# Kernel tuning notes

Measured on AMD Instinct MI355X. Metric: run time of the kernel, lower is better.

## Reference

```python
import jax, jax.numpy as jnp
import numpy as np

HID = 64
L = 5
N_NODES = 50000
N_EDGES = 1600000
N_GRAPHS = 4
EPS = 1e-5


def _ln(h, g, b):
    m = jnp.mean(h, axis=-1, keepdims=True)
    v = jnp.mean((h - m) ** 2, axis=-1, keepdims=True)
    return (h - m) * jax.lax.rsqrt(v + EPS) * g + b


def _lin_init(key, fan_in, fan_out):
    return jax.random.normal(key, (fan_in, fan_out), jnp.float32) / np.sqrt(fan_in)


def setup_inputs() -> dict:
    key = jax.random.key(0)
    ks = jax.random.split(key, 24)
    inp = {}
    inp['x'] = jax.random.normal(ks[0], (N_NODES, 8), jnp.float32)
    inp['edge_index'] = jax.random.randint(ks[1], (2, N_EDGES), 0, N_NODES)
    inp['edge_attr'] = jax.random.normal(ks[2], (N_EDGES, 5), jnp.float32)
    inp['batch'] = jnp.sort(jax.random.randint(ks[3], (N_NODES,), 0, N_GRAPHS))
    inp['case_params'] = jax.random.normal(ks[4], (N_GRAPHS, 4), jnp.float32)
    inp['bc_params'] = jax.random.normal(ks[5], (N_GRAPHS, 4), jnp.float32)
    # encoder
    inp['enc_W1'] = _lin_init(ks[6], 16, HID); inp['enc_b1'] = jnp.zeros((HID,))
    inp['enc_W2'] = _lin_init(ks[7], HID, HID); inp['enc_b2'] = jnp.zeros((HID,))
    inp['enc_g'] = jnp.ones((HID,)); inp['enc_be'] = jnp.zeros((HID,))
    # processor (stacked over L layers)
    ek = jax.random.split(ks[8], L); nk = jax.random.split(ks[9], L)
    ek2 = jax.random.split(ks[10], L); nk2 = jax.random.split(ks[11], L)
    inp['eW1'] = jnp.stack([_lin_init(ek[i], 2 * HID + 5, HID) for i in range(L)])
    inp['eb1'] = jnp.zeros((L, HID))
    inp['eW2'] = jnp.stack([_lin_init(ek2[i], HID, HID) for i in range(L)])
    inp['eb2'] = jnp.zeros((L, HID))
    inp['eg'] = jnp.ones((L, HID)); inp['ebe'] = jnp.zeros((L, HID))
    inp['nW1'] = jnp.stack([_lin_init(nk[i], 2 * HID, HID) for i in range(L)])
    inp['nb1'] = jnp.zeros((L, HID))
    inp['nW2'] = jnp.stack([_lin_init(nk2[i], HID, HID) for i in range(L)])
    inp['nb2'] = jnp.zeros((L, HID))
    inp['ng'] = jnp.ones((L, HID)); inp['nbe'] = jnp.zeros((L, HID))
    # decoders
    inp['dlW1'] = _lin_init(ks[12], HID, HID); inp['dlb1'] = jnp.zeros((HID,))
    inp['dlW2'] = _lin_init(ks[13], HID, 6); inp['dlb2'] = jnp.zeros((6,))
    inp['dgW1'] = _lin_init(ks[14], HID, HID // 2); inp['dgb1'] = jnp.zeros((HID // 2,))
    inp['dgW2'] = _lin_init(ks[15], HID // 2, 4); inp['dgb2'] = jnp.zeros((4,))
    return inp


def reference(x, edge_index, edge_attr, batch, case_params, bc_params,
              enc_W1, enc_b1, enc_W2, enc_b2, enc_g, enc_be,
              eW1, eb1, eW2, eb2, eg, ebe,
              nW1, nb1, nW2, nb2, ng, nbe,
              dlW1, dlb1, dlW2, dlb2, dgW1, dgb1, dgW2, dgb2):
    n_nodes = x.shape[0]
    n_graphs = case_params.shape[0]
    silu = jax.nn.silu
    # input concat: node feats + per-graph globals gathered by batch index
    gv = jnp.concatenate([case_params, bc_params], axis=1)  # [B, 8]
    h = jnp.concatenate([x, gv[batch]], axis=1)             # [N, 16]
    # encoder
    h = _ln(silu(h @ enc_W1 + enc_b1) @ enc_W2 + enc_b2, enc_g, enc_be)
    src, dst = edge_index[0], edge_index[1]  # PyG: x_j = src, x_i = dst
    n_layers = eW1.shape[0]
    for l in range(n_layers):
        xi = h[dst]  # [E, H] target
        xj = h[src]  # [E, H] source
        m = jnp.concatenate([xi, xj, edge_attr], axis=1)  # [E, 2H+5]
        m = _ln(silu(m @ eW1[l] + eb1[l]) @ eW2[l] + eb2[l], eg[l], ebe[l])
        agg = jax.ops.segment_sum(m, dst, num_segments=n_nodes)  # scatter-add
        t = jnp.concatenate([h, agg], axis=1)  # [N, 2H]
        h = h + _ln(silu(t @ nW1[l] + nb1[l]) @ nW2[l] + nb2[l], ng[l], nbe[l])
    out_local = silu(h @ dlW1 + dlb1) @ dlW2 + dlb2  # [N, 6]
    cnt = jax.ops.segment_sum(jnp.ones((n_nodes,), h.dtype), batch, num_segments=n_graphs)
    pooled = jax.ops.segment_sum(h, batch, num_segments=n_graphs) / jnp.maximum(cnt, 1.0)[:, None]
    out_global = silu(pooled @ dgW1 + dgb1) @ dgW2 + dgb2  # [B, 4]
    return (out_local, out_global)
```

## Files before the change

kernel.cpp:

```cpp
#include <hip/hip_runtime.h>
#include <cmath>

constexpr int NN = 50000;
constexpr int NE = 1600000;
constexpr int H  = 64;
constexpr int NL = 5;
constexpr int NG = 4;
constexpr int EIN = 2 * H + 5;
constexpr int NIN = 2 * H;

typedef short bf16x8 __attribute__((ext_vector_type(8)));
typedef float f32x4  __attribute__((ext_vector_type(4)));

__device__ __forceinline__ float silu_f(float x) {
    return x / (1.0f + __expf(-x));
}

__device__ __forceinline__ unsigned int f2bf(float f) {
    unsigned int u = __float_as_uint(f);
    u += 0x7fffu + ((u >> 16) & 1u);
    return u >> 16;
}
__device__ __forceinline__ unsigned int pack_bf16x2(float x, float y) {
    unsigned int r;
    asm("v_cvt_pk_bf16_f32 %0, %1, %2" : "=v"(r) : "v"(x), "v"(y));
    return r;
}

template <int CTRL>
__device__ __forceinline__ int dpp_i(int old, int v) {
    return __builtin_amdgcn_update_dpp(old, v, CTRL, 0xF, 0xF, false);
}

__global__ __launch_bounds__(256) void degree_kernel(
    const int* __restrict__ ei, int* __restrict__ deg)
{
    int e = blockIdx.x * 256 + threadIdx.x;
    if (e < NE) atomicAdd(&deg[ei[NE + e]], 1);
}

__global__ __launch_bounds__(1024) void scan1_kernel(
    const int* __restrict__ deg, int* __restrict__ off, int* __restrict__ bsum)
{
    __shared__ int sh[1024];
    const int tid = threadIdx.x;
    int i = blockIdx.x * 1024 + tid;
    int v = (i < NN) ? deg[i] : 0;
    sh[tid] = v;
    __syncthreads();
    for (int d = 1; d < 1024; d <<= 1) {
        int t = (tid >= d) ? sh[tid - d] : 0;
        __syncthreads();
        sh[tid] += t;
        __syncthreads();
    }
    if (i < NN) off[i] = sh[tid] - v;
    if (tid == 1023) bsum[blockIdx.x] = sh[1023];
}

__global__ __launch_bounds__(64) void scan2_kernel(
    const int* __restrict__ bsum, int* __restrict__ bbase, int nb)
{
    int lane = threadIdx.x;
    int v = (lane < nb) ? bsum[lane] : 0;
    int orig = v;
    for (int d = 1; d < 64; d <<= 1) {
        int t = __shfl_up(v, d);
        if (lane >= d) v += t;
    }
    bbase[lane] = v - orig;
}

__global__ __launch_bounds__(1024) void scan3_kernel(
    int* __restrict__ off, const int* __restrict__ bbase,
    int* __restrict__ cursor)
{
    int i = blockIdx.x * 1024 + threadIdx.x;
    if (i < NN) {
        int o = off[i] + bbase[blockIdx.x];
        off[i] = o;
        cursor[i] = o;
        if (i == NN - 1) off[NN] = NE;
    }
}

__global__ __launch_bounds__(256) void scatter_kernel(
    const int* __restrict__ ei, int* __restrict__ cursor,
    int* __restrict__ sidx, int* __restrict__ sdst, int* __restrict__ ssrc)
{
    int e = blockIdx.x * 256 + threadIdx.x;
    if (e < NE) {
        int d = ei[NE + e];
        int p = atomicAdd(&cursor[d], 1);
        sidx[p] = e;
        sdst[p] = d;
        ssrc[p] = ei[e];
    }
}

__global__ __launch_bounds__(256) void ea_pack_kernel(
    const float* __restrict__ ea, const int* __restrict__ sidx,
    uint4* __restrict__ ea_pk)
{
    int p = blockIdx.x * 256 + threadIdx.x;
    if (p < NE) {
        const float* s = ea + (size_t)sidx[p] * 5;
        uint4 v;
        v.x = pack_bf16x2(s[0], s[1]);
        v.y = pack_bf16x2(s[2], s[3]);
        v.z = pack_bf16x2(s[4], 0.0f);
        v.w = 0u;
        ea_pk[p] = v;
    }
}

__global__ __launch_bounds__(256) void pack_weights_kernel(
    const float* __restrict__ eW1, const float* __restrict__ eW2,
    const float* __restrict__ nW1, const float* __restrict__ nW2,
    const float* __restrict__ dlW1, const float* __restrict__ dlW2,
    short* __restrict__ eW1pk, short* __restrict__ eW2pk,
    short* __restrict__ nW1pk, short* __restrict__ nW2pk,
    short* __restrict__ dlW1pk, short* __restrict__ dlW2pk)
{
    int l = blockIdx.y;
    int t = blockIdx.x * 256 + threadIdx.x;
    if (t < 10240) {
        int j = t & 7, lane = (t >> 3) & 63, mt = (t >> 9) & 3, ks = t >> 11;
        int k  = ks * 32 + (lane >> 4) * 8 + j;
        int ch = mt * 16 + (lane & 15);
        float v = (k < EIN) ? eW1[(size_t)l * EIN * H + k * H + ch] : 0.0f;
        eW1pk[(size_t)l * 10240 + t] = (short)f2bf(v);
    } else if (t < 14336) {
        int t2 = t - 10240;
        int j = t2 & 7, lane = (t2 >> 3) & 63, mt = (t2 >> 9) & 3, ks = t2 >> 11;
        int k = ks * 32 + (lane >> 4) * 8 + j;
        int ch = mt * 16 + (lane & 15);
        eW2pk[(size_t)l * 4096 + t2] = (short)f2bf(eW2[(size_t)l * H * H + k * H + ch]);
    } else if (t < 22528) {
        int t3 = t - 14336;
        int j = t3 & 7, lane = (t3 >> 3) & 63, mt = (t3 >> 9) & 3, ks = t3 >> 11;
        int k = ks * 32 + (lane >> 4) * 8 + j;
        int ch = mt * 16 + (lane & 15);
        nW1pk[(size_t)l * 8192 + t3] = (short)f2bf(nW1[(size_t)l * NIN * H + k * H + ch]);
    } else if (t < 26624) {
        int t4 = t - 22528;
        int j = t4 & 7, lane = (t4 >> 3) & 63, mt = (t4 >> 9) & 3, ks = t4 >> 11;
        int k = ks * 32 + (lane >> 4) * 8 + j;
        int ch = mt * 16 + (lane & 15);
        nW2pk[(size_t)l * 4096 + t4] = (short)f2bf(nW2[(size_t)l * H * H + k * H + ch]);
    } else if (t < 30720) {
        if (l == 0) {
            int t5 = t - 26624;
            int j = t5 & 7, lane = (t5 >> 3) & 63, mt = (t5 >> 9) & 3, ks = t5 >> 11;
            int k = ks * 32 + (lane >> 4) * 8 + j;
            int ch = mt * 16 + (lane & 15);
            dlW1pk[t5] = (short)f2bf(dlW1[k * H + ch]);
        }
    } else if (t < 31744) {
        if (l == 0) {
            int t6 = t - 30720;
            int j = t6 & 7, lane = (t6 >> 3) & 63, ks = t6 >> 9;
            int k = ks * 32 + (lane >> 4) * 8 + j;
            int m = lane & 15;
            float v = (m < 6) ? dlW2[k * 6 + m] : 0.0f;
            dlW2pk[t6] = (short)f2bf(v);
        }
    }
}

__global__ __launch_bounds__(256) void encoder_kernel(
    const float* __restrict__ x, const int* __restrict__ batch,
    const float* __restrict__ case_p, const float* __restrict__ bc_p,
    const float* __restrict__ W1, const float* __restrict__ b1,
    const float* __restrict__ W2, const float* __restrict__ b2,
    const float* __restrict__ g, const float* __restrict__ be,
    float* __restrict__ h, unsigned int* __restrict__ h2)
{
    __shared__ float in_sh[64 * 17];
    __shared__ float m1_sh[64 * 65];
    __shared__ float red_sh[2 * 4 * 64];
    const int lane = threadIdx.x & 63;
    const int w    = threadIdx.x >> 6;
    const int wb   = __builtin_amdgcn_readfirstlane(w * 16);
    const int n0   = blockIdx.x * 64;

    for (int i = 0; i < 16; ++i) {
        int slot = w * 16 + i;
        int n = n0 + slot;
        if (n < NN && lane < 16) {
            float v;
            if (lane < 8) v = x[n * 8 + lane];
            else {
                int b = batch[n];
                v = (lane < 12) ? case_p[b * 4 + (lane - 8)]
                                : bc_p[b * 4 + (lane - 12)];
            }
            in_sh[slot * 17 + lane] = v;
        }
    }
    __syncthreads();

    float acc[16];
#pragma unroll
    for (int c = 0; c < 16; ++c) acc[c] = b1[wb + c];
    for (int k = 0; k < 16; ++k) {
        float a = in_sh[lane * 17 + k];
        const float4* wr = (const float4*)(W1 + k * 64 + wb);
        float4 w0 = wr[0], w1 = wr[1], w2 = wr[2], w3 = wr[3];
        acc[0]  = fmaf(a, w0.x, acc[0]);  acc[1]  = fmaf(a, w0.y, acc[1]);
        acc[2]  = fmaf(a, w0.z, acc[2]);  acc[3]  = fmaf(a, w0.w, acc[3]);
        acc[4]  = fmaf(a, w1.x, acc[4]);  acc[5]  = fmaf(a, w1.y, acc[5]);
        acc[6]  = fmaf(a, w1.z, acc[6]);  acc[7]  = fmaf(a, w1.w, acc[7]);
        acc[8]  = fmaf(a, w2.x, acc[8]);  acc[9]  = fmaf(a, w2.y, acc[9]);
        acc[10] = fmaf(a, w2.z, acc[10]); acc[11] = fmaf(a, w2.w, acc[11]);
        acc[12] = fmaf(a, w3.x, acc[12]); acc[13] = fmaf(a, w3.y, acc[13]);
        acc[14] = fmaf(a, w3.z, acc[14]); acc[15] = fmaf(a, w3.w, acc[15]);
    }
#pragma unroll
    for (int c = 0; c < 16; ++c) m1_sh[lane * 65 + wb + c] = silu_f(acc[c]);
    __syncthreads();

    float acc2[16];
#pragma unroll
    for (int c = 0; c < 16; ++c) acc2[c] = b2[wb + c];
    for (int k = 0; k < 64; ++k) {
        float a = m1_sh[lane * 65 + k];
        const float4* wr = (const float4*)(W2 + k * 64 + wb);
        float4 w0 = wr[0], w1 = wr[1], w2 = wr[2], w3 = wr[3];
        acc2[0]  = fmaf(a, w0.x, acc2[0]);  acc2[1]  = fmaf(a, w0.y, acc2[1]);
        acc2[2]  = fmaf(a, w0.z, acc2[2]);  acc2[3]  = fmaf(a, w0.w, acc2[3]);
        acc2[4]  = fmaf(a, w1.x, acc2[4]);  acc2[5]  = fmaf(a, w1.y, acc2[5]);
        acc2[6]  = fmaf(a, w1.z, acc2[6]);  acc2[7]  = fmaf(a, w1.w, acc2[7]);
        acc2[8]  = fmaf(a, w2.x, acc2[8]);  acc2[9]  = fmaf(a, w2.y, acc2[9]);
        acc2[10] = fmaf(a, w2.z, acc2[10]); acc2[11] = fmaf(a, w2.w, acc2[11]);
        acc2[12] = fmaf(a, w3.x, acc2[12]); acc2[13] = fmaf(a, w3.y, acc2[13]);
        acc2[14] = fmaf(a, w3.z, acc2[14]); acc2[15] = fmaf(a, w3.w, acc2[15]);
    }

    float s1 = 0.f, s2 = 0.f;
#pragma unroll
    for (int c = 0; c < 16; ++c) { s1 += acc2[c]; s2 += acc2[c] * acc2[c]; }
    red_sh[w * 64 + lane] = s1;
    red_sh[256 + w * 64 + lane] = s2;
    __syncthreads();
    float t1 = 0.f, t2 = 0.f;
#pragma unroll
    for (int j = 0; j < 4; ++j) {
        t1 += red_sh[j * 64 + lane];
        t2 += red_sh[256 + j * 64 + lane];
    }
    float mean = t1 * (1.0f / 64.0f);
    float var  = t2 * (1.0f / 64.0f) - mean * mean;
    float rstd = rsqrtf(var + 1e-5f);

    int n = n0 + lane;
    if (n < NN) {
        float vals[16];
#pragma unroll
        for (int c = 0; c < 16; ++c) {
            int ch = wb + c;
            vals[c] = (acc2[c] - mean) * rstd * g[ch] + be[ch];
            h[n * 64 + ch] = vals[c];
        }
        uint4 p0, p1;
        p0.x = pack_bf16x2(vals[0], vals[1]);   p0.y = pack_bf16x2(vals[2], vals[3]);
        p0.z = pack_bf16x2(vals[4], vals[5]);   p0.w = pack_bf16x2(vals[6], vals[7]);
        p1.x = pack_bf16x2(vals[8], vals[9]);   p1.y = pack_bf16x2(vals[10], vals[11]);
        p1.z = pack_bf16x2(vals[12], vals[13]); p1.w = pack_bf16x2(vals[14], vals[15]);
        *(uint4*)(h2 + (size_t)n * 32 + w * 8)     = p0;
        *(uint4*)(h2 + (size_t)n * 32 + w * 8 + 4) = p1;
    }
}

__global__ __launch_bounds__(256, 7) void edge_kernel(
    const unsigned int* __restrict__ h2,
    const int* __restrict__ sdst, const int* __restrict__ ssrc,
    const uint4* __restrict__ ea_pk,
    const short* __restrict__ W1pk, const float* __restrict__ b1,
    const short* __restrict__ W2pk, const float* __restrict__ b2,
    const float* __restrict__ g, const float* __restrict__ be,
    float* __restrict__ agg)
{
    __shared__ unsigned int lds[4 * 576];
    const int lane = threadIdx.x & 63;
    const int w    = threadIdx.x >> 6;
    const int quad = lane >> 4;
    const int l15  = lane & 15;
    const int tile = (blockIdx.x & 7) * 3125 + (blockIdx.x >> 3);
    const int e0   = tile * 64 + w * 16;
    unsigned int* MID = lds + w * 576;

    const int d_l = sdst[e0 + l15];
    const int s_l = ssrc[e0 + l15];

    union { uint4 u; bf16x8 b; } eacv;
    eacv.u = ea_pk[e0 + l15];
    const bf16x8 zfrag = {0, 0, 0, 0, 0, 0, 0, 0};
    const bf16x8 ks4frag = (quad == 0) ? eacv.b : zfrag;

    const unsigned int* drow = h2 + (size_t)d_l * 32 + quad * 4;
    const unsigned int* srow = h2 + (size_t)s_l * 32 + quad * 4;
    union { uint4 u; bf16x8 b; } bfA, bfB, bfC, bfD;
    bfA.u = *(const uint4*)(drow);
    bfB.u = *(const uint4*)(drow + 16);
    bfC.u = *(const uint4*)(srow);
    bfD.u = *(const uint4*)(srow + 16);

    f32x4 acc1[4] = {{0,0,0,0},{0,0,0,0},{0,0,0,0},{0,0,0,0}};
#define G1_STEP(KS, BFRAG)                                                    \
    {                                                                         \
        const short* apk = W1pk + (size_t)((KS) * 4) * 512 + lane * 8;        \
        _Pragma("unroll")                                                     \
        for (int mt = 0; mt < 4; ++mt) {                                      \
            bf16x8 afrag = *(const bf16x8*)(apk + mt * 512);                  \
            acc1[mt] = __builtin_amdgcn_mfma_f32_16x16x32_bf16(               \
                afrag, BFRAG, acc1[mt], 0, 0, 0);                             \
        }                                                                     \
    }
    G1_STEP(0, bfA.b)
    G1_STEP(1, bfB.b)
    G1_STEP(2, bfC.b)
    G1_STEP(3, bfD.b)
    G1_STEP(4, ks4frag)
#undef G1_STEP

#pragma unroll
    for (int mt = 0; mt < 4; ++mt) {
        int ch0 = mt * 16 + quad * 4;
        float v0 = silu_f(acc1[mt][0] + b1[ch0 + 0]);
        float v1 = silu_f(acc1[mt][1] + b1[ch0 + 1]);
        float v2 = silu_f(acc1[mt][2] + b1[ch0 + 2]);
        float v3 = silu_f(acc1[mt][3] + b1[ch0 + 3]);
        uint2 pk;
        pk.x = pack_bf16x2(v0, v1);
        pk.y = pack_bf16x2(v2, v3);
        *(uint2*)(MID + l15 * 36 + mt * 8 + quad * 2) = pk;
    }

    f32x4 acc2[4] = {{0,0,0,0},{0,0,0,0},{0,0,0,0},{0,0,0,0}};
    const unsigned int* mrow = MID + l15 * 36;
    for (int ks = 0; ks < 2; ++ks) {
        bf16x8 bfrag = *(const bf16x8*)(mrow + ks * 16 + quad * 4);
        const short* apk = W2pk + (size_t)(ks * 4) * 512 + lane * 8;
#pragma unroll
        for (int mt = 0; mt < 4; ++mt) {
            bf16x8 afrag = *(const bf16x8*)(apk + mt * 512);
            acc2[mt] = __builtin_amdgcn_mfma_f32_16x16x32_bf16(
                afrag, bfrag, acc2[mt], 0, 0, 0);
        }
    }

    float vals[16];
    float s1 = 0.f, s2 = 0.f;
#pragma unroll
    for (int mt = 0; mt < 4; ++mt) {
#pragma unroll
        for (int r = 0; r < 4; ++r) {
            int ch = mt * 16 + quad * 4 + r;
            float vv = acc2[mt][r] + b2[ch];
            vals[mt * 4 + r] = vv;
            s1 += vv; s2 += vv * vv;
        }
    }
    s1 += __shfl_xor(s1, 16); s1 += __shfl_xor(s1, 32);
    s2 += __shfl_xor(s2, 16); s2 += __shfl_xor(s2, 32);
    float mean = s1 * (1.0f / 64.0f);
    float var  = s2 * (1.0f / 64.0f) - mean * mean;
    float rstd = rsqrtf(var + 1e-5f);
#pragma unroll
    for (int mt = 0; mt < 4; ++mt) {
#pragma unroll
        for (int r = 0; r < 4; ++r) {
            int ch = mt * 16 + quad * 4 + r;
            vals[mt * 4 + r] = (vals[mt * 4 + r] - mean) * rstd * g[ch] + be[ch];
        }
    }

#define SEG_STEP(CTRL)                                                        \
    {                                                                         \
        int d_up = dpp_i<CTRL>(-1, d_l);                                      \
        float msk = (d_up == d_l) ? 1.0f : 0.0f;                              \
        _Pragma("unroll")                                                     \
        for (int c = 0; c < 16; ++c) {                                        \
            float vu = __int_as_float(dpp_i<CTRL>(0, __float_as_int(vals[c])));\
            vals[c] = fmaf(vu, msk, vals[c]);                                 \
        }                                                                     \
    }
    SEG_STEP(0x111)
    SEG_STEP(0x112)
    SEG_STEP(0x114)
    SEG_STEP(0x118)
#undef SEG_STEP
    int d_next = dpp_i<0x101>(-1, d_l);
    bool last = (d_next != d_l);
    if (last) {
#pragma unroll
        for (int mt = 0; mt < 4; ++mt) {
#pragma unroll
            for (int r = 0; r < 4; ++r) {
                int ch = mt * 16 + quad * 4 + r;
                atomicAdd(&agg[(size_t)d_l * 64 + ch], vals[mt * 4 + r]);
            }
        }
    }
}

__global__ __launch_bounds__(256, 6) void node_kernel(
    float* __restrict__ h, unsigned int* __restrict__ h2,
    const float* __restrict__ agg,
    const short* __restrict__ W1pk, const float* __restrict__ b1,
    const short* __restrict__ W2pk, const float* __restrict__ b2,
    const float* __restrict__ g, const float* __restrict__ be)
{
    __shared__ unsigned int lds[4 * 576];
    const int lane = threadIdx.x & 63;
    const int w    = threadIdx.x >> 6;
    const int quad = lane >> 4;
    const int l15  = lane & 15;
    const int n0   = blockIdx.x * 64 + w * 16;
    unsigned int* MID = lds + w * 576;

    int n_l = n0 + l15; if (n_l >= NN) n_l = NN - 1;

    const unsigned int* nrow = h2 + (size_t)n_l * 32 + quad * 4;
    union { uint4 u; bf16x8 b; } bfA, bfB;
    bfA.u = *(const uint4*)(nrow);
    bfB.u = *(const uint4*)(nrow + 16);
    const float* ap = agg + (size_t)n_l * 64 + quad * 8;
    float4 a0 = *(const float4*)(ap);
    float4 a1 = *(const float4*)(ap + 4);
    float4 a2 = *(const float4*)(ap + 32);
    float4 a3 = *(const float4*)(ap + 36);
    union { unsigned int u[4]; bf16x8 b; } bfC, bfD;
    bfC.u[0] = pack_bf16x2(a0.x, a0.y); bfC.u[1] = pack_bf16x2(a0.z, a0.w);
    bfC.u[2] = pack_bf16x2(a1.x, a1.y); bfC.u[3] = pack_bf16x2(a1.z, a1.w);
    bfD.u[0] = pack_bf16x2(a2.x, a2.y); bfD.u[1] = pack_bf16x2(a2.z, a2.w);
    bfD.u[2] = pack_bf16x2(a3.x, a3.y); bfD.u[3] = pack_bf16x2(a3.z, a3.w);

    f32x4 acc1[4] = {{0,0,0,0},{0,0,0,0},{0,0,0,0},{0,0,0,0}};
#define G1_STEP(KS, BFRAG)                                                    \
    {                                                                         \
        const short* apk = W1pk + (size_t)((KS) * 4) * 512 + lane * 8;        \
        _Pragma("unroll")                                                     \
        for (int mt = 0; mt < 4; ++mt) {                                      \
            bf16x8 afrag = *(const bf16x8*)(apk + mt * 512);                  \
            acc1[mt] = __builtin_amdgcn_mfma_f32_16x16x32_bf16(               \
                afrag, BFRAG, acc1[mt], 0, 0, 0);                             \
        }                                                                     \
    }
    G1_STEP(0, bfA.b)
    G1_STEP(1, bfB.b)
    G1_STEP(2, bfC.b)
    G1_STEP(3, bfD.b)
#undef G1_STEP

#pragma unroll
    for (int mt = 0; mt < 4; ++mt) {
        int ch0 = mt * 16 + quad * 4;
        float v0 = silu_f(acc1[mt][0] + b1[ch0 + 0]);
        float v1 = silu_f(acc1[mt][1] + b1[ch0 + 1]);
        float v2 = silu_f(acc1[mt][2] + b1[ch0 + 2]);
        float v3 = silu_f(acc1[mt][3] + b1[ch0 + 3]);
        uint2 pk;
        pk.x = pack_bf16x2(v0, v1);
        pk.y = pack_bf16x2(v2, v3);
        *(uint2*)(MID + l15 * 36 + mt * 8 + quad * 2) = pk;
    }

    f32x4 acc2[4] = {{0,0,0,0},{0,0,0,0},{0,0,0,0},{0,0,0,0}};
    const unsigned int* mrow = MID + l15 * 36;
    for (int ks = 0; ks < 2; ++ks) {
        bf16x8 bfrag = *(const bf16x8*)(mrow + ks * 16 + quad * 4);
        const short* apk = W2pk + (size_t)(ks * 4) * 512 + lane * 8;
#pragma unroll
        for (int mt = 0; mt < 4; ++mt) {
            bf16x8 afrag = *(const bf16x8*)(apk + mt * 512);
            acc2[mt] = __builtin_amdgcn_mfma_f32_16x16x32_bf16(
                afrag, bfrag, acc2[mt], 0, 0, 0);
        }
    }

    float vals[16];
    float s1 = 0.f, s2 = 0.f;
#pragma unroll
    for (int mt = 0; mt < 4; ++mt) {
#pragma unroll
        for (int r = 0; r < 4; ++r) {
            int ch = mt * 16 + quad * 4 + r;
            float vv = acc2[mt][r] + b2[ch];
            vals[mt * 4 + r] = vv;
            s1 += vv; s2 += vv * vv;
        }
    }
    s1 += __shfl_xor(s1, 16); s1 += __shfl_xor(s1, 32);
    s2 += __shfl_xor(s2, 16); s2 += __shfl_xor(s2, 32);
    float mean = s1 * (1.0f / 64.0f);
    float var  = s2 * (1.0f / 64.0f) - mean * mean;
    float rstd = rsqrtf(var + 1e-5f);

    int n = n0 + l15;
    if (n < NN) {
#pragma unroll
        for (int mt = 0; mt < 4; ++mt) {
            int ch0 = mt * 16 + quad * 4;
            float4 hv = *(const float4*)(h + (size_t)n * 64 + ch0);
            float o0 = hv.x + (vals[mt*4+0] - mean) * rstd * g[ch0+0] + be[ch0+0];
            float o1 = hv.y + (vals[mt*4+1] - mean) * rstd * g[ch0+1] + be[ch0+1];
            float o2 = hv.z + (vals[mt*4+2] - mean) * rstd * g[ch0+2] + be[ch0+2];
            float o3 = hv.w + (vals[mt*4+3] - mean) * rstd * g[ch0+3] + be[ch0+3];
            float4 st = {o0, o1, o2, o3};
            *(float4*)(h + (size_t)n * 64 + ch0) = st;
            uint2 pk;
            pk.x = pack_bf16x2(o0, o1);
            pk.y = pack_bf16x2(o2, o3);
            *(uint2*)(h2 + (size_t)n * 32 + mt * 8 + quad * 2) = pk;
        }
    }
}

__global__ __launch_bounds__(256, 7) void dec_local_kernel(
    const unsigned int* __restrict__ h2,
    const short* __restrict__ W1pk, const float* __restrict__ b1,
    const short* __restrict__ W2pk, const float* __restrict__ b2,
    float* __restrict__ out)
{
    __shared__ unsigned int lds[4 * 576];
    const int lane = threadIdx.x & 63;
    const int w    = threadIdx.x >> 6;
    const int quad = lane >> 4;
    const int l15  = lane & 15;
    const int n0   = blockIdx.x * 64 + w * 16;
    unsigned int* MID = lds + w * 576;

    int n_l = n0 + l15; if (n_l >= NN) n_l = NN - 1;
    const unsigned int* nrow = h2 + (size_t)n_l * 32 + quad * 4;
    union { uint4 u; bf16x8 b; } bfA, bfB;
    bfA.u = *(const uint4*)(nrow);
    bfB.u = *(const uint4*)(nrow + 16);

    f32x4 acc1[4] = {{0,0,0,0},{0,0,0,0},{0,0,0,0},{0,0,0,0}};
#define G1_STEP(KS, BFRAG)                                                    \
    {                                                                         \
        const short* apk = W1pk + (size_t)((KS) * 4) * 512 + lane * 8;        \
        _Pragma("unroll")                                                     \
        for (int mt = 0; mt < 4; ++mt) {                                      \
            bf16x8 afrag = *(const bf16x8*)(apk + mt * 512);                  \
            acc1[mt] = __builtin_amdgcn_mfma_f32_16x16x32_bf16(               \
                afrag, BFRAG, acc1[mt], 0, 0, 0);                             \
        }                                                                     \
    }
    G1_STEP(0, bfA.b)
    G1_STEP(1, bfB.b)
#undef G1_STEP

#pragma unroll
    for (int mt = 0; mt < 4; ++mt) {
        int ch0 = mt * 16 + quad * 4;
        float v0 = silu_f(acc1[mt][0] + b1[ch0 + 0]);
        float v1 = silu_f(acc1[mt][1] + b1[ch0 + 1]);
        float v2 = silu_f(acc1[mt][2] + b1[ch0 + 2]);
        float v3 = silu_f(acc1[mt][3] + b1[ch0 + 3]);
        uint2 pk;
        pk.x = pack_bf16x2(v0, v1);
        pk.y = pack_bf16x2(v2, v3);
        *(uint2*)(MID + l15 * 36 + mt * 8 + quad * 2) = pk;
    }

    f32x4 acc2 = {0, 0, 0, 0};
    const unsigned int* mrow = MID + l15 * 36;
    for (int ks = 0; ks < 2; ++ks) {
        bf16x8 bfrag = *(const bf16x8*)(mrow + ks * 16 + quad * 4);
        bf16x8 afrag = *(const bf16x8*)(W2pk + (size_t)ks * 512 + lane * 8);
        acc2 = __builtin_amdgcn_mfma_f32_16x16x32_bf16(afrag, bfrag, acc2, 0, 0, 0);
    }

    int n = n0 + l15;
    if (n < NN && quad < 2) {
#pragma unroll
        for (int r = 0; r < 4; ++r) {
            int ch = quad * 4 + r;
            if (ch < 6) out[(size_t)n * 6 + ch] = acc2[r] + b2[ch];
        }
    }
}

__global__ __launch_bounds__(256) void pool_kernel(
    const float* __restrict__ h, const int* __restrict__ batch,
    float* __restrict__ pooled, float* __restrict__ cnt)
{
    const int c   = threadIdx.x & 63;
    const int rep = blockIdx.x * 4 + (threadIdx.x >> 6);
    float acc[NG] = {0.f, 0.f, 0.f, 0.f};
    float cl[NG]  = {0.f, 0.f, 0.f, 0.f};
    for (int n = rep; n < NN; n += 1024) {
        int b = batch[n];
        float v = h[n * 64 + c];
#pragma unroll
        for (int gph = 0; gph < NG; ++gph) {
            if (b == gph) { acc[gph] += v; cl[gph] += 1.0f; }
        }
    }
#pragma unroll
    for (int gph = 0; gph < NG; ++gph) {
        atomicAdd(&pooled[gph * 64 + c], acc[gph]);
        if (c == 0) atomicAdd(&cnt[gph], cl[gph]);
    }
}

__global__ __launch_bounds__(256) void dec_global_kernel(
    const float* __restrict__ pooled, const float* __restrict__ cnt,
    const float* __restrict__ W1, const float* __restrict__ b1,
    const float* __restrict__ W2, const float* __restrict__ b2,
    float* __restrict__ out)
{
    __shared__ float mid_sh[4][32];
    const int lane = threadIdx.x & 63;
    const int gph  = threadIdx.x >> 6;
    float inv = 1.0f / fmaxf(cnt[gph], 1.0f);
    if (lane < 32) {
        float a = b1[lane];
        for (int k = 0; k < 64; ++k)
            a = fmaf(pooled[gph * 64 + k] * inv, W1[k * 32 + lane], a);
        mid_sh[gph][lane] = silu_f(a);
    }
    __syncthreads();
    if (lane < 4) {
        float o = b2[lane];
        for (int k = 0; k < 32; ++k)
            o = fmaf(mid_sh[gph][k], W2[k * 4 + lane], o);
        out[gph * 4 + lane] = o;
    }
}

extern "C" void kernel_launch(void* const* d_in, const int* in_sizes, int n_in,
                              void* d_out, int out_size, void* d_ws, size_t ws_size,
                              hipStream_t stream)
{
    const float* x      = (const float*)d_in[0];
    const int*   ei     = (const int*)  d_in[1];
    const float* ea     = (const float*)d_in[2];
    const int*   batch  = (const int*)  d_in[3];
    const float* case_p = (const float*)d_in[4];
    const float* bc_p   = (const float*)d_in[5];
    const float* enc_W1 = (const float*)d_in[6];
    const float* enc_b1 = (const float*)d_in[7];
    const float* enc_W2 = (const float*)d_in[8];
    const float* enc_b2 = (const float*)d_in[9];
    const float* enc_g  = (const float*)d_in[10];
    const float* enc_be = (const float*)d_in[11];
    const float* eW1    = (const float*)d_in[12];
    const float* eb1    = (const float*)d_in[13];
    const float* eW2    = (const float*)d_in[14];
    const float* eb2    = (const float*)d_in[15];
    const float* eg     = (const float*)d_in[16];
    const float* ebe    = (const float*)d_in[17];
    const float* nW1    = (const float*)d_in[18];
    const float* nb1    = (const float*)d_in[19];
    const float* nW2    = (const float*)d_in[20];
    const float* nb2    = (const float*)d_in[21];
    const float* ng     = (const float*)d_in[22];
    const float* nbe    = (const float*)d_in[23];
    const float* dlW1   = (const float*)d_in[24];
    const float* dlb1   = (const float*)d_in[25];
    const float* dlW2   = (const float*)d_in[26];
    const float* dlb2   = (const float*)d_in[27];
    const float* dgW1   = (const float*)d_in[28];
    const float* dgb1   = (const float*)d_in[29];
    const float* dgW2   = (const float*)d_in[30];
    const float* dgb2   = (const float*)d_in[31];

    float* out = (float*)d_out;

    char* ws = (char*)d_ws;
    size_t off_b = 0;
    auto alloc = [&](size_t bytes) {
        void* p = ws + off_b;
        off_b = (off_b + bytes + 255) & ~(size_t)255;
        return p;
    };
    const size_t hBytes = (size_t)NN * H * sizeof(float);
    float*        h      = (float*)alloc(hBytes);
    float*        agg    = (float*)alloc(hBytes);
    unsigned int* h2     = (unsigned int*)alloc((size_t)NN * 32 * 4);
    float*        pooled = (float*)alloc(256 * sizeof(float));
    float*        cnt    = (float*)alloc(4 * sizeof(float));
    int*          deg    = (int*)alloc((NN + 1) * sizeof(int));
    int*          offs   = (int*)alloc((NN + 1) * sizeof(int));
    int*          cursor = (int*)alloc((NN + 1) * sizeof(int));
    int*          bsum   = (int*)alloc(64 * sizeof(int));
    int*          bbase  = (int*)alloc(64 * sizeof(int));
    int*          sidx   = (int*)alloc((size_t)NE * sizeof(int));
    int*          sdst   = (int*)alloc((size_t)NE * sizeof(int));
    int*          ssrc   = (int*)alloc((size_t)NE * sizeof(int));
    uint4*        ea_pk  = (uint4*)alloc((size_t)NE * sizeof(uint4));
    short*        eW1pk  = (short*)alloc((size_t)NL * 10240 * sizeof(short));
    short*        eW2pk  = (short*)alloc((size_t)NL * 4096 * sizeof(short));
    short*        nW1pk  = (short*)alloc((size_t)NL * 8192 * sizeof(short));
    short*        nW2pk  = (short*)alloc((size_t)NL * 4096 * sizeof(short));
    short*        dlW1pk = (short*)alloc(4096 * sizeof(short));
    short*        dlW2pk = (short*)alloc(1024 * sizeof(short));

    hipMemsetAsync(pooled, 0, (256 + 4 + 64) * sizeof(float), stream);
    hipMemsetAsync(deg, 0, (NN + 1) * sizeof(int), stream);

    const int NB = (NN + 1023) / 1024;
    degree_kernel<<<(NE + 255) / 256, 256, 0, stream>>>(ei, deg);
    scan1_kernel<<<NB, 1024, 0, stream>>>(deg, offs, bsum);
    scan2_kernel<<<1, 64, 0, stream>>>(bsum, bbase, NB);
    scan3_kernel<<<NB, 1024, 0, stream>>>(offs, bbase, cursor);
    scatter_kernel<<<(NE + 255) / 256, 256, 0, stream>>>(ei, cursor, sidx, sdst, ssrc);
    ea_pack_kernel<<<(NE + 255) / 256, 256, 0, stream>>>(ea, sidx, ea_pk);
    pack_weights_kernel<<<dim3(124, NL), 256, 0, stream>>>(
        eW1, eW2, nW1, nW2, dlW1, dlW2,
        eW1pk, eW2pk, nW1pk, nW2pk, dlW1pk, dlW2pk);

    const int nodeBlocks = (NN + 63) / 64;
    encoder_kernel<<<nodeBlocks, 256, 0, stream>>>(
        x, batch, case_p, bc_p, enc_W1, enc_b1, enc_W2, enc_b2, enc_g, enc_be,
        h, h2);

    for (int l = 0; l < NL; ++l) {
        hipMemsetAsync(agg, 0, hBytes, stream);
        edge_kernel<<<NE / 64, 256, 0, stream>>>(
            h2, sdst, ssrc, ea_pk,
            eW1pk + (size_t)l * 10240, eb1 + l * H,
            eW2pk + (size_t)l * 4096,  eb2 + l * H,
            eg + l * H, ebe + l * H, agg);
        node_kernel<<<nodeBlocks, 256, 0, stream>>>(
            h, h2, agg,
            nW1pk + (size_t)l * 8192, nb1 + l * H,
            nW2pk + (size_t)l * 4096, nb2 + l * H,
            ng + l * H, nbe + l * H);
    }

    dec_local_kernel<<<nodeBlocks, 256, 0, stream>>>(
        h2, dlW1pk, dlb1, dlW2pk, dlb2, out);
    pool_kernel<<<256, 256, 0, stream>>>(h, batch, pooled, cnt);
    dec_global_kernel<<<1, 256, 0, stream>>>(pooled, cnt, dgW1, dgb1, dgW2, dgb2,
                                             out + (size_t)NN * 6);
}
```

Baseline: 1.590 ms.

## Stage edge/node MLP weights in LDS and make edge kernel persistent

The edge kernel now launches 800 blocks of 512 threads. Each block first copies the packed W1/W2 weights, biases and LayerNorm params into LDS, then loops its 8 waves over 125 sixteen-edge tiles, instead of launching one block per 64 edges that reads weights from global memory. The node kernel gets the same LDS staging with 512-thread blocks covering 128 nodes. The aim is to cut repeated global/L2 weight-fragment loads for the MFMA A-operands and spread the staging cost over many tiles. In exchange it uses about 37KB of LDS per block, which may limit occupancy, and adds a block-level sync.

```diff
diff --git a/kernel.cpp b/kernel.cpp
--- a/kernel.cpp
+++ b/kernel.cpp
@@ -272,7 +272,7 @@
     }
 }
 
-__global__ __launch_bounds__(256, 7) void edge_kernel(
+__global__ __launch_bounds__(512, 6) void edge_kernel(
     const unsigned int* __restrict__ h2,
     const int* __restrict__ sdst, const int* __restrict__ ssrc,
     const uint4* __restrict__ ea_pk,
@@ -281,145 +281,199 @@
     const float* __restrict__ g, const float* __restrict__ be,
     float* __restrict__ agg)
 {
-    __shared__ unsigned int lds[4 * 576];
-    const int lane = threadIdx.x & 63;
-    const int w    = threadIdx.x >> 6;
+    __shared__ uint4 w1s4[1280];
+    __shared__ uint4 w2s4[512];
+    __shared__ float b1s[64], b2s[64], gs[64], bes[64];
+    __shared__ unsigned int mids[8 * 576];
+
+    const int tid  = threadIdx.x;
+    const int lane = tid & 63;
+    const int w    = tid >> 6;
     const int quad = lane >> 4;
     const int l15  = lane & 15;
-    const int tile = (blockIdx.x & 7) * 3125 + (blockIdx.x >> 3);
-    const int e0   = tile * 64 + w * 16;
-    unsigned int* MID = lds + w * 576;
-
-    const int d_l = sdst[e0 + l15];
-    const int s_l = ssrc[e0 + l15];
-
-    union { uint4 u; bf16x8 b; } eacv;
-    eacv.u = ea_pk[e0 + l15];
+
+    {
+        const uint4* s1 = (const uint4*)W1pk;
+        for (int i = tid; i < 1280; i += 512) w1s4[i] = s1[i];
+        const uint4* s2 = (const uint4*)W2pk;
+        w2s4[tid] = s2[tid];
+        if (tid < 64) {
+            b1s[tid] = b1[tid];
+            b2s[tid] = b2[tid];
+            gs[tid]  = g[tid];
+            bes[tid] = be[tid];
+        }
+    }
+    __syncthreads();
+
+    const short* w1s = (const short*)w1s4;
+    const short* w2s = (const short*)w2s4;
+    unsigned int* MID = mids + w * 576;
     const bf16x8 zfrag = {0, 0, 0, 0, 0, 0, 0, 0};
-    const bf16x8 ks4frag = (quad == 0) ? eacv.b : zfrag;
-
-    const unsigned int* drow = h2 + (size_t)d_l * 32 + quad * 4;
-    const unsigned int* srow = h2 + (size_t)s_l * 32 + quad * 4;
-    union { uint4 u; bf16x8 b; } bfA, bfB, bfC, bfD;
-    bfA.u = *(const uint4*)(drow);
-    bfB.u = *(const uint4*)(drow + 16);
-    bfC.u = *(const uint4*)(srow);
-    bfD.u = *(const uint4*)(srow + 16);
-
-    f32x4 acc1[4] = {{0,0,0,0},{0,0,0,0},{0,0,0,0},{0,0,0,0}};
+
+    const int blk   = (blockIdx.x & 7) * 100 + (blockIdx.x >> 3);
+    const int wbase = blk * 125;
+
+    for (int W = wbase + w; W < wbase + 125; W += 8) {
+        const int eI = W * 16 + l15;
+        const int d_l = sdst[eI];
+        const int s_l = ssrc[eI];
+        union { uint4 u; bf16x8 b; } eacv;
+        eacv.u = ea_pk[eI];
+        bf16x8 ks4frag = (quad == 0) ? eacv.b : zfrag;
+
+        const unsigned int* drow = h2 + (size_t)d_l * 32 + quad * 4;
+        const unsigned int* srow = h2 + (size_t)s_l * 32 + quad * 4;
+        union { uint4 u; bf16x8 b; } bfA, bfB, bfC, bfD;
+        bfA.u = *(const uint4*)(drow);
+        bfB.u = *(const uint4*)(drow + 16);
+        bfC.u = *(const uint4*)(srow);
+        bfD.u = *(const uint4*)(srow + 16);
+
+        f32x4 acc1[4] = {{0,0,0,0},{0,0,0,0},{0,0,0,0},{0,0,0,0}};
 #define G1_STEP(KS, BFRAG)                                                    \
-    {                                                                         \
-        const short* apk = W1pk + (size_t)((KS) * 4) * 512 + lane * 8;        \
-        _Pragma("unroll")                                                     \
-        for (int mt = 0; mt < 4; ++mt) {                                      \
-            bf16x8 afrag = *(const bf16x8*)(apk + mt * 512);                  \
-            acc1[mt] = __builtin_amdgcn_mfma_f32_16x16x32_bf16(               \
-                afrag, BFRAG, acc1[mt], 0, 0, 0);                             \
-        }                                                                     \
-    }
-    G1_STEP(0, bfA.b)
-    G1_STEP(1, bfB.b)
-    G1_STEP(2, bfC.b)
-    G1_STEP(3, bfD.b)
-    G1_STEP(4, ks4frag)
+        {                                                                     \
+            const short* apk = w1s + (KS) * 4 * 512 + lane * 8;               \
+            _Pragma("unroll")                                                 \
+            for (int mt = 0; mt < 4; ++mt) {                                  \
+                bf16x8 afrag = *(const bf16x8*)(apk + mt * 512);              \
+                acc1[mt] = __builtin_amdgcn_mfma_f32_16x16x32_bf16(           \
+                    afrag, BFRAG, acc1[mt], 0, 0, 0);                         \
+            }                                                                 \
+        }
+        G1_STEP(0, bfA.b)
+        G1_STEP(1, bfB.b)
+        G1_STEP(2, bfC.b)
+        G1_STEP(3, bfD.b)
+        G1_STEP(4, ks4frag)
 #undef G1_STEP
 
 #pragma unroll
-    for (int mt = 0; mt < 4; ++mt) {
-        int ch0 = mt * 16 + quad * 4;
-        float v0 = silu_f(acc1[mt][0] + b1[ch0 + 0]);
-        float v1 = silu_f(acc1[mt][1] + b1[ch0 + 1]);
-        float v2 = silu_f(acc1[mt][2] + b1[ch0 + 2]);
-        float v3 = silu_f(acc1[mt][3] + b1[ch0 + 3]);
-        uint2 pk;
-        pk.x = pack_bf16x2(v0, v1);
-        pk.y = pack_bf16x2(v2, v3);
-        *(uint2*)(MID + l15 * 36 + mt * 8 + quad * 2) = pk;
-    }
-
-    f32x4 acc2[4] = {{0,0,0,0},{0,0,0,0},{0,0,0,0},{0,0,0,0}};
-    const unsigned int* mrow = MID + l15 * 36;
-    for (int ks = 0; ks < 2; ++ks) {
-        bf16x8 bfrag = *(const bf16x8*)(mrow + ks * 16 + quad * 4);
-        const short* apk = W2pk + (size_t)(ks * 4) * 512 + lane * 8;
-#pragma unroll
         for (int mt = 0; mt < 4; ++mt) {
-            bf16x8 afrag = *(const bf16x8*)(apk + mt * 512);
-            acc2[mt] = __builtin_amdgcn_mfma_f32_16x16x32_bf16(
-                afrag, bfrag, acc2[mt], 0, 0, 0);
-        }
-    }
-
-    float vals[16];
-    float s1 = 0.f, s2 = 0.f;
-#pragma unroll
-    for (int mt = 0; mt < 4; ++mt) {
-#pragma unroll
-        for (int r = 0; r < 4; ++r) {
-            int ch = mt * 16 + quad * 4 + r;
-            float vv = acc2[mt][r] + b2[ch];
-            vals[mt * 4 + r] = vv;
-            s1 += vv; s2 += vv * vv;
-        }
-    }
-    s1 += __shfl_xor(s1, 16); s1 += __shfl_xor(s1, 32);
-    s2 += __shfl_xor(s2, 16); s2 += __shfl_xor(s2, 32);
-    float mean = s1 * (1.0f / 64.0f);
-    float var  = s2 * (1.0f / 64.0f) - mean * mean;
-    float rstd = rsqrtf(var + 1e-5f);
-#pragma unroll
-    for (int mt = 0; mt < 4; ++mt) {
-#pragma unroll
-        for (int r = 0; r < 4; ++r) {
-            int ch = mt * 16 + quad * 4 + r;
-            vals[mt * 4 + r] = (vals[mt * 4 + r] - mean) * rstd * g[ch] + be[ch];
-        }
-    }
+            int ch0 = mt * 16 + quad * 4;
+            float4 bb1 = *(const float4*)(&b1s[ch0]);
+            float v0 = silu_f(acc1[mt][0] + bb1.x);
+            float v1 = silu_f(acc1[mt][1] + bb1.y);
+            float v2 = silu_f(acc1[mt][2] + bb1.z);
+            float v3 = silu_f(acc1[mt][3] + bb1.w);
+            uint2 pk;
+            pk.x = pack_bf16x2(v0, v1);
+            pk.y = pack_bf16x2(v2, v3);
+            *(uint2*)(MID + l15 * 36 + mt * 8 + quad * 2) = pk;
+        }
+
+        f32x4 acc2[4] = {{0,0,0,0},{0,0,0,0},{0,0,0,0},{0,0,0,0}};
+        const unsigned int* mrow = MID + l15 * 36;
+#pragma unroll
+        for (int ks = 0; ks < 2; ++ks) {
+            bf16x8 bfrag = *(const bf16x8*)(mrow + ks * 16 + quad * 4);
+            const short* apk = w2s + ks * 4 * 512 + lane * 8;
+#pragma unroll
+            for (int mt = 0; mt < 4; ++mt) {
+                bf16x8 afrag = *(const bf16x8*)(apk + mt * 512);
+                acc2[mt] = __builtin_amdgcn_mfma_f32_16x16x32_bf16(
+                    afrag, bfrag, acc2[mt], 0, 0, 0);
+            }
+        }
+
+        float vals[16];
+        float s1 = 0.f, s2 = 0.f;
+#pragma unroll
+        for (int mt = 0; mt < 4; ++mt) {
+            int ch0 = mt * 16 + quad * 4;
+            float4 bb2 = *(const float4*)(&b2s[ch0]);
+#pragma unroll
+            for (int r = 0; r < 4; ++r) {
+                float vv = acc2[mt][r] +
+                           (r == 0 ? bb2.x : r == 1 ? bb2.y : r == 2 ? bb2.z : bb2.w);
+                vals[mt * 4 + r] = vv;
+                s1 += vv; s2 += vv * vv;
+            }
+        }
+        s1 += __shfl_xor(s1, 16); s1 += __shfl_xor(s1, 32);
+        s2 += __shfl_xor(s2, 16); s2 += __shfl_xor(s2, 32);
+        float mean = s1 * (1.0f / 64.0f);
+        float var  = s2 * (1.0f / 64.0f) - mean * mean;
+        float rstd = rsqrtf(var + 1e-5f);
+#pragma unroll
+        for (int mt = 0; mt < 4; ++mt) {
+            int ch0 = mt * 16 + quad * 4;
+            float4 gg  = *(const float4*)(&gs[ch0]);
+            float4 bbe = *(const float4*)(&bes[ch0]);
+            vals[mt*4+0] = (vals[mt*4+0] - mean) * rstd * gg.x + bbe.x;
+            vals[mt*4+1] = (vals[mt*4+1] - mean) * rstd * gg.y + bbe.y;
+            vals[mt*4+2] = (vals[mt*4+2] - mean) * rstd * gg.z + bbe.z;
+            vals[mt*4+3] = (vals[mt*4+3] - mean) * rstd * gg.w + bbe.w;
+        }
 
 #define SEG_STEP(CTRL)                                                        \
-    {                                                                         \
-        int d_up = dpp_i<CTRL>(-1, d_l);                                      \
-        float msk = (d_up == d_l) ? 1.0f : 0.0f;                              \
-        _Pragma("unroll")                                                     \
-        for (int c = 0; c < 16; ++c) {                                        \
-            float vu = __int_as_float(dpp_i<CTRL>(0, __float_as_int(vals[c])));\
-            vals[c] = fmaf(vu, msk, vals[c]);                                 \
-        }                                                                     \
-    }
-    SEG_STEP(0x111)
-    SEG_STEP(0x112)
-    SEG_STEP(0x114)
-    SEG_STEP(0x118)
+        {                                                                     \
+            int d_up = dpp_i<CTRL>(-1, d_l);                                  \
+            float msk = (d_up == d_l) ? 1.0f : 0.0f;                          \
+            _Pragma("unroll")                                                 \
+            for (int c = 0; c < 16; ++c) {                                    \
+                float vu = __int_as_float(                                    \
+                    dpp_i<CTRL>(0, __float_as_int(vals[c])));                 \
+                vals[c] = fmaf(vu, msk, vals[c]);                             \
+            }                                                                 \
+        }
+        SEG_STEP(0x111)
+        SEG_STEP(0x112)
+        SEG_STEP(0x114)
+        SEG_STEP(0x118)
 #undef SEG_STEP
-    int d_next = dpp_i<0x101>(-1, d_l);
-    bool last = (d_next != d_l);
-    if (last) {
-#pragma unroll
-        for (int mt = 0; mt < 4; ++mt) {
-#pragma unroll
-            for (int r = 0; r < 4; ++r) {
-                int ch = mt * 16 + quad * 4 + r;
-                atomicAdd(&agg[(size_t)d_l * 64 + ch], vals[mt * 4 + r]);
+        int d_next = dpp_i<0x101>(-1, d_l);
+        bool last = (d_next != d_l);
+        if (last) {
+#pragma unroll
+            for (int mt = 0; mt < 4; ++mt) {
+#pragma unroll
+                for (int r = 0; r < 4; ++r) {
+                    int ch = mt * 16 + quad * 4 + r;
+                    atomicAdd(&agg[(size_t)d_l * 64 + ch], vals[mt * 4 + r]);
+                }
             }
         }
     }
 }
 
-__global__ __launch_bounds__(256, 6) void node_kernel(
+__global__ __launch_bounds__(512, 6) void node_kernel(
     float* __restrict__ h, unsigned int* __restrict__ h2,
     const float* __restrict__ agg,
     const short* __restrict__ W1pk, const float* __restrict__ b1,
     const short* __restrict__ W2pk, const float* __restrict__ b2,
     const float* __restrict__ g, const float* __restrict__ be)
 {
-    __shared__ unsigned int lds[4 * 576];
-    const int lane = threadIdx.x & 63;
-    const int w    = threadIdx.x >> 6;
+    __shared__ uint4 w1s4[1024];
+    __shared__ uint4 w2s4[512];
+    __shared__ float b1s[64], b2s[64], gs[64], bes[64];
+    __shared__ unsigned int mids[8 * 576];
+
+    const int tid  = threadIdx.x;
+    const int lane = tid & 63;
+    const int w    = tid >> 6;
     const int quad = lane >> 4;
     const int l15  = lane & 15;
-    const int n0   = blockIdx.x * 64 + w * 16;
-    unsigned int* MID = lds + w * 576;
-
+
+    {
+        const uint4* s1 = (const uint4*)W1pk;
+        for (int i = tid; i < 1024; i += 512) w1s4[i] = s1[i];
+        const uint4* s2 = (const uint4*)W2pk;
+        w2s4[tid] = s2[tid];
+        if (tid < 64) {
+            b1s[tid] = b1[tid];
+            b2s[tid] = b2[tid];
+            gs[tid]  = g[tid];
+            bes[tid] = be[tid];
+        }
+    }
+    __syncthreads();
+
+    const short* w1s = (const short*)w1s4;
+    const short* w2s = (const short*)w2s4;
+    unsigned int* MID = mids + w * 576;
+
+    const int n0 = blockIdx.x * 128 + w * 16;
     int n_l = n0 + l15; if (n_l >= NN) n_l = NN - 1;
 
     const unsigned int* nrow = h2 + (size_t)n_l * 32 + quad * 4;
@@ -440,7 +494,7 @@
     f32x4 acc1[4] = {{0,0,0,0},{0,0,0,0},{0,0,0,0},{0,0,0,0}};
 #define G1_STEP(KS, BFRAG)                                                    \
     {                                                                         \
-        const short* apk = W1pk + (size_t)((KS) * 4) * 512 + lane * 8;        \
+        const short* apk = w1s + (KS) * 4 * 512 + lane * 8;                   \
         _Pragma("unroll")                                                     \
         for (int mt = 0; mt < 4; ++mt) {                                      \
             bf16x8 afrag = *(const bf16x8*)(apk + mt * 512);                  \
@@ -457,10 +511,11 @@
 #pragma unroll
     for (int mt = 0; mt < 4; ++mt) {
         int ch0 = mt * 16 + quad * 4;
-        float v0 = silu_f(acc1[mt][0] + b1[ch0 + 0]);
-        float v1 = silu_f(acc1[mt][1] + b1[ch0 + 1]);
-        float v2 = silu_f(acc1[mt][2] + b1[ch0 + 2]);
-        float v3 = silu_f(acc1[mt][3] + b1[ch0 + 3]);
+        float4 bb1 = *(const float4*)(&b1s[ch0]);
+        float v0 = silu_f(acc1[mt][0] + bb1.x);
+        float v1 = silu_f(acc1[mt][1] + bb1.y);
+        float v2 = silu_f(acc1[mt][2] + bb1.z);
+        float v3 = silu_f(acc1[mt][3] + bb1.w);
         uint2 pk;
         pk.x = pack_bf16x2(v0, v1);
         pk.y = pack_bf16x2(v2, v3);
@@ -469,9 +524,10 @@
 
     f32x4 acc2[4] = {{0,0,0,0},{0,0,0,0},{0,0,0,0},{0,0,0,0}};
     const unsigned int* mrow = MID + l15 * 36;
+#pragma unroll
     for (int ks = 0; ks < 2; ++ks) {
         bf16x8 bfrag = *(const bf16x8*)(mrow + ks * 16 + quad * 4);
-        const short* apk = W2pk + (size_t)(ks * 4) * 512 + lane * 8;
+        const short* apk = w2s + ks * 4 * 512 + lane * 8;
 #pragma unroll
         for (int mt = 0; mt < 4; ++mt) {
             bf16x8 afrag = *(const bf16x8*)(apk + mt * 512);
@@ -484,10 +540,12 @@
     float s1 = 0.f, s2 = 0.f;
 #pragma unroll
     for (int mt = 0; mt < 4; ++mt) {
+        int ch0 = mt * 16 + quad * 4;
+        float4 bb2 = *(const float4*)(&b2s[ch0]);
 #pragma unroll
         for (int r = 0; r < 4; ++r) {
-            int ch = mt * 16 + quad * 4 + r;
-            float vv = acc2[mt][r] + b2[ch];
+            float vv = acc2[mt][r] +
+                       (r == 0 ? bb2.x : r == 1 ? bb2.y : r == 2 ? bb2.z : bb2.w);
             vals[mt * 4 + r] = vv;
             s1 += vv; s2 += vv * vv;
         }
@@ -503,11 +561,13 @@
 #pragma unroll
         for (int mt = 0; mt < 4; ++mt) {
             int ch0 = mt * 16 + quad * 4;
+            float4 gg  = *(const float4*)(&gs[ch0]);
+            float4 bbe = *(const float4*)(&bes[ch0]);
             float4 hv = *(const float4*)(h + (size_t)n * 64 + ch0);
-            float o0 = hv.x + (vals[mt*4+0] - mean) * rstd * g[ch0+0] + be[ch0+0];
-            float o1 = hv.y + (vals[mt*4+1] - mean) * rstd * g[ch0+1] + be[ch0+1];
-            float o2 = hv.z + (vals[mt*4+2] - mean) * rstd * g[ch0+2] + be[ch0+2];
-            float o3 = hv.w + (vals[mt*4+3] - mean) * rstd * g[ch0+3] + be[ch0+3];
+            float o0 = hv.x + (vals[mt*4+0] - mean) * rstd * gg.x + bbe.x;
+            float o1 = hv.y + (vals[mt*4+1] - mean) * rstd * gg.y + bbe.y;
+            float o2 = hv.z + (vals[mt*4+2] - mean) * rstd * gg.z + bbe.z;
+            float o3 = hv.w + (vals[mt*4+3] - mean) * rstd * gg.w + bbe.w;
             float4 st = {o0, o1, o2, o3};
             *(float4*)(h + (size_t)n * 64 + ch0) = st;
             uint2 pk;
@@ -719,14 +779,16 @@
         x, batch, case_p, bc_p, enc_W1, enc_b1, enc_W2, enc_b2, enc_g, enc_be,
         h, h2);
 
+    const int edgeBlocks  = 800;
+    const int node2Blocks = (NN + 127) / 128;
     for (int l = 0; l < NL; ++l) {
         hipMemsetAsync(agg, 0, hBytes, stream);
-        edge_kernel<<<NE / 64, 256, 0, stream>>>(
+        edge_kernel<<<edgeBlocks, 512, 0, stream>>>(
             h2, sdst, ssrc, ea_pk,
             eW1pk + (size_t)l * 10240, eb1 + l * H,
             eW2pk + (size_t)l * 4096,  eb2 + l * H,
             eg + l * H, ebe + l * H, agg);
-        node_kernel<<<nodeBlocks, 256, 0, stream>>>(
+        node_kernel<<<node2Blocks, 512, 0, stream>>>(
             h, h2, agg,
             nW1pk + (size_t)l * 8192, nb1 + l * H,
             nW2pk + (size_t)l * 4096, nb2 + l * H,
```

New measurement: 2.685 ms. 1.69x slower.
